# Performance work log

Hardware: AMD Instinct MI355X
Metric: run time of the kernel (lower is better)

The kernel has to match this reference:

```python
import jax, jax.numpy as jnp
import numpy as np

B, L, ENC, EMB, H, V = 64, 33, 512, 256, 512, 32000


def setup_inputs() -> dict:
    key = jax.random.key(0)
    ks = jax.random.split(key, 16)
    x = jax.random.normal(ks[0], (B, ENC), dtype=jnp.float32)
    padded_target = jax.random.randint(ks[1], (B, L), 0, V)
    target_lengths = jax.random.randint(ks[2], (B,), 2, L + 1)
    target_lengths = target_lengths.at[0].set(L)  # pin max length -> static step count
    s = 0.05
    return {
        "x": x,
        "padded_target": padded_target,
        "target_lengths": target_lengths,
        "embed": jax.random.normal(ks[3], (V, EMB), dtype=jnp.float32) * s,
        "W_h0": jax.random.normal(ks[4], (H, ENC), dtype=jnp.float32) * s,
        "b_h0": jnp.zeros((H,), jnp.float32),
        "W_c0": jax.random.normal(ks[5], (H, ENC), dtype=jnp.float32) * s,
        "b_c0": jnp.zeros((H,), jnp.float32),
        "W_ih": jax.random.normal(ks[6], (4 * H, ENC + EMB), dtype=jnp.float32) * s,
        "W_hh": jax.random.normal(ks[7], (4 * H, H), dtype=jnp.float32) * s,
        "b_ih": jnp.zeros((4 * H,), jnp.float32),
        "b_hh": jnp.zeros((4 * H,), jnp.float32),
        "W_out": jax.random.normal(ks[8], (V, H), dtype=jnp.float32) * s,
        "b_out": jnp.zeros((V,), jnp.float32),
    }


def reference(x, padded_target, target_lengths, embed, W_h0, b_h0, W_c0, b_c0,
              W_ih, W_hh, b_ih, b_hh, W_out, b_out):
    # sort by length, descending (packed-sequence ordering)
    sorted_indices = jnp.argsort(-target_lengths)
    x = x[sorted_indices]                      # [B, ENC]
    tgt = padded_target[sorted_indices]        # [B, L]
    lens = target_lengths[sorted_indices] - 1  # decode steps per row
    emb = embed[tgt]                           # [B, L, EMB]

    h = x @ W_h0.T + b_h0                      # context-initialized state
    c = x @ W_c0.T + b_c0
    T = padded_target.shape[1] - 1             # static max steps (max len pinned to L)

    def step(carry, inp):
        h, c = carry
        e_t, t = inp
        active = (lens > t)[:, None]           # rows still decoding (prefix, sorted)
        g = jnp.concatenate([x, e_t], axis=1) @ W_ih.T + b_ih + h @ W_hh.T + b_hh
        i, f, gg, o = jnp.split(g, 4, axis=1)  # torch LSTMCell gate order i,f,g,o
        c_new = jax.nn.sigmoid(f) * c + jax.nn.sigmoid(i) * jnp.tanh(gg)
        h_new = jax.nn.sigmoid(o) * jnp.tanh(c_new)
        h = jnp.where(active, h_new, h)        # inactive rows keep frozen state
        c = jnp.where(active, c_new, c)
        pred = jnp.where(active, h_new @ W_out.T + b_out, 0.0)  # dropout p=0
        return (h, c), pred

    (_, _), preds = jax.lax.scan(
        step, (h, c), (jnp.transpose(emb[:, :T], (1, 0, 2)), jnp.arange(T)))
    prediction = jnp.transpose(preds, (1, 0, 2))  # [B, T, V]
    return prediction, sorted_indices
```

## Files before the change

kernel.cpp:

```cpp
#include <hip/hip_runtime.h>

typedef __attribute__((ext_vector_type(8))) short short8;
typedef __attribute__((ext_vector_type(8))) unsigned short ushort8;
typedef __attribute__((ext_vector_type(4))) float f32x4;
typedef __attribute__((ext_vector_type(4))) unsigned short ushort4v;

#define DEV __device__ __forceinline__

DEV unsigned short f2bf(float f) {
  unsigned int u = __float_as_uint(f);
  u += 0x7fffu + ((u >> 16) & 1u);
  return (unsigned short)(u >> 16);
}
DEV float sigm(float x) { return 1.f / (1.f + __expf(-x)); }
DEV float tanh_(float x) { return 1.f - 2.f / (1.f + __expf(2.f * x)); }

typedef __attribute__((address_space(1))) const void* as1cv;
typedef __attribute__((address_space(3))) void* as3v;
DEV void gll16(const void* g, void* l) {
  __builtin_amdgcn_global_load_lds((as1cv)g, (as3v)l, 16, 0, 0);
}

__global__ void __launch_bounds__(256) k_sort(const float* __restrict__ x,
    const int* __restrict__ ptar, const int* __restrict__ tlen,
    int* __restrict__ sidx, int* __restrict__ lens, int* __restrict__ tok,
    float* __restrict__ xs, float* __restrict__ tail) {
  __shared__ int ss[64];
  int tid = threadIdx.x;
  if (tid < 64) {
    int li = tlen[tid];
    int rank = 0;
    for (int j = 0; j < 64; ++j) {
      int lj = tlen[j];
      rank += (lj > li || (lj == li && j < tid)) ? 1 : 0;
    }
    ss[rank] = tid;
  }
  __syncthreads();
  if (tid < 64) {
    int src = ss[tid];
    sidx[tid] = src;
    lens[tid] = tlen[src] - 1;
    tail[tid] = (float)src;
  }
  __syncthreads();
  for (int idx = tid; idx < 32 * 64; idx += 256) {
    int t = idx >> 6, b = idx & 63;
    tok[idx] = ptar[ss[b] * 33 + t];
  }
  for (int idx = tid; idx < 64 * 512; idx += 256) {
    int b = idx >> 9;
    xs[idx] = x[ss[b] * 512 + (idx & 511)];
  }
}

__global__ void __launch_bounds__(256) k_convmany(
    const float* __restrict__ W_h0, const float* __restrict__ W_c0,
    const float* __restrict__ W_ih, const float* __restrict__ W_hh,
    const float* __restrict__ xs,
    unsigned short* __restrict__ Wpro, unsigned short* __restrict__ Wihb2,
    unsigned short* __restrict__ Whb, unsigned short* __restrict__ xsb) {
  long long g = (long long)(blockIdx.x * 256 + threadIdx.x) * 8;
  const float* src;
  unsigned short* dst;
  if (g < 262144) {
    src = W_h0 + g; dst = Wpro + g;
  } else if (g < 524288) {
    long long l = g - 262144; src = W_c0 + l; dst = Wpro + 262144 + l;
  } else if (g < 1572864) {
    long long l = g - 524288;
    long long r = l >> 9, c = l & 511;
    src = W_ih + r * 768 + c; dst = Wpro + 524288 + l;
  } else if (g < 2097152) {
    long long l = g - 1572864;
    long long r = l >> 8, c = l & 255;
    src = W_ih + r * 768 + 512 + c; dst = Wihb2 + l;
  } else if (g < 3145728) {
    long long l = g - 2097152; src = W_hh + l; dst = Whb + l;
  } else {
    long long l = g - 3145728; src = xs + l; dst = xsb + l;
  }
  float4 v0 = *(const float4*)src, v1 = *(const float4*)(src + 4);
  ushort8 o;
  o[0] = f2bf(v0.x); o[1] = f2bf(v0.y); o[2] = f2bf(v0.z); o[3] = f2bf(v0.w);
  o[4] = f2bf(v1.x); o[5] = f2bf(v1.y); o[6] = f2bf(v1.z); o[7] = f2bf(v1.w);
  *(ushort8*)dst = o;
}

__global__ void __launch_bounds__(256) k_conv(const float* __restrict__ W,
    unsigned short* __restrict__ Wb) {
  size_t i = (size_t)(blockIdx.x * 256 + threadIdx.x) * 4;
  float4 v = *(const float4*)(W + i);
  ushort4v o;
  o.x = f2bf(v.x); o.y = f2bf(v.y); o.z = f2bf(v.z); o.w = f2bf(v.w);
  *(ushort4v*)(Wb + i) = o;
}

__global__ void __launch_bounds__(256) k_pro(const unsigned short* __restrict__ xsb,
    const unsigned short* __restrict__ Wpro, const float* __restrict__ b_h0,
    const float* __restrict__ b_c0, const float* __restrict__ b_ih,
    const float* __restrict__ b_hh, unsigned short* __restrict__ h0b,
    float* __restrict__ c, float* __restrict__ gx) {
  int tid = threadIdx.x, lane = tid & 63, w = tid >> 6;
  int n0 = blockIdx.x * 64 + w * 16;
  int lr = lane & 15, lk = lane >> 4;
  f32x4 acc[4];
#pragma unroll
  for (int i = 0; i < 4; ++i) acc[i] = (f32x4){0.f, 0.f, 0.f, 0.f};
  const unsigned short* B = Wpro + (size_t)(n0 + lr) * 512 + lk * 8;
  const unsigned short* A = xsb + (size_t)lr * 512 + lk * 8;
#pragma unroll
  for (int ks = 0; ks < 16; ++ks) {
    short8 bfr = *(const short8*)(B + ks * 32);
#pragma unroll
    for (int mi = 0; mi < 4; ++mi) {
      short8 af = *(const short8*)(A + mi * 16 * 512 + ks * 32);
      acc[mi] = __builtin_amdgcn_mfma_f32_16x16x32_bf16(af, bfr, acc[mi], 0, 0, 0);
    }
  }
  int n = n0 + lr;
#pragma unroll
  for (int mi = 0; mi < 4; ++mi)
#pragma unroll
    for (int r = 0; r < 4; ++r) {
      int b = mi * 16 + lk * 4 + r;
      float v = acc[mi][r];
      if (n < 512) {
        h0b[b * 512 + n] = f2bf(v + b_h0[n]);
      } else if (n < 1024) {
        int u = n - 512;
        c[b * 512 + u] = v + b_c0[u];
      } else {
        int j = n - 1024;
        gx[(size_t)b * 2048 + j] = v + b_ih[j] + b_hh[j];
      }
    }
}

__global__ void __launch_bounds__(256) k_emb(const int* __restrict__ tok,
    const float* __restrict__ embed, unsigned short* __restrict__ Eb) {
  int gid = blockIdx.x * 256 + threadIdx.x;
  int row = gid >> 5, c8 = (gid & 31) * 8;
  const float* src = embed + (size_t)tok[row] * 256 + c8;
  float4 v0 = *(const float4*)src, v1 = *(const float4*)(src + 4);
  ushort8 o;
  o[0] = f2bf(v0.x); o[1] = f2bf(v0.y); o[2] = f2bf(v0.z); o[3] = f2bf(v0.w);
  o[4] = f2bf(v1.x); o[5] = f2bf(v1.y); o[6] = f2bf(v1.z); o[7] = f2bf(v1.w);
  *(ushort8*)(Eb + (size_t)row * 256 + c8) = o;
}

__global__ void __launch_bounds__(256) k_ga2(const unsigned short* __restrict__ Eb,
    const unsigned short* __restrict__ Wb2, const float* __restrict__ gx,
    float* __restrict__ GA) {
  __shared__ alignas(16) char ldsbuf[32768];
  char* ldsA = ldsbuf;
  char* ldsB = ldsbuf + 16384;
  int bid = blockIdx.x;
  int mt = bid & 15, nt = bid >> 4;
  int m0 = mt * 128, n0 = nt * 128;
  int tid = threadIdx.x, lane = tid & 63, w = tid >> 6;
  int wm = w >> 1, wn = w & 1;
  f32x4 acc[4][4];
#pragma unroll
  for (int a = 0; a < 4; ++a)
#pragma unroll
    for (int bq = 0; bq < 4; ++bq) acc[a][bq] = (f32x4){0.f, 0.f, 0.f, 0.f};
  const unsigned short* Arow = Eb + (size_t)m0 * 256;
  const unsigned short* Brow = Wb2 + (size_t)n0 * 256;
  for (int kt = 0; kt < 4; ++kt) {
    int k0 = kt * 64;
    if (kt) __syncthreads();
#pragma unroll
    for (int j = 0; j < 4; ++j) {
      int ci = j * 256 + w * 64 + lane;
      int r = ci >> 3;
      int clog = ((ci & 7) << 4) ^ ((r & 7) << 4);
      int ldst = (j * 256 + w * 64) * 16;
      gll16((const char*)(Arow + (size_t)r * 256 + k0) + clog, ldsA + ldst);
      gll16((const char*)(Brow + (size_t)r * 256 + k0) + clog, ldsB + ldst);
    }
    __syncthreads();
#pragma unroll
    for (int kk = 0; kk < 2; ++kk) {
      short8 af[4], bf[4];
      int cb = kk * 64 + (lane >> 4) * 16;
#pragma unroll
      for (int i = 0; i < 4; ++i) {
        int ar = wm * 64 + i * 16 + (lane & 15);
        af[i] = *(const short8*)(ldsA + ar * 128 + (cb ^ ((ar & 7) << 4)));
        int br = wn * 64 + i * 16 + (lane & 15);
        bf[i] = *(const short8*)(ldsB + br * 128 + (cb ^ ((br & 7) << 4)));
      }
#pragma unroll
      for (int mi = 0; mi < 4; ++mi)
#pragma unroll
        for (int ni = 0; ni < 4; ++ni)
          acc[mi][ni] = __builtin_amdgcn_mfma_f32_16x16x32_bf16(
              af[mi], bf[ni], acc[mi][ni], 0, 0, 0);
    }
  }
#pragma unroll
  for (int mi = 0; mi < 4; ++mi) {
    int mb = m0 + wm * 64 + mi * 16 + ((lane >> 4) << 2);
#pragma unroll
    for (int r = 0; r < 4; ++r) {
      int m = mb + r;
#pragma unroll
      for (int ni = 0; ni < 4; ++ni) {
        int j = n0 + wn * 64 + ni * 16 + (lane & 15);
        GA[(size_t)m * 2048 + j] = acc[mi][ni][r] + gx[(size_t)(m & 63) * 2048 + j];
      }
    }
  }
}

__global__ void __launch_bounds__(256) k_step2(
    const unsigned short* __restrict__ hin, unsigned short* __restrict__ hout,
    float* __restrict__ c, const float* __restrict__ GA,
    const unsigned short* __restrict__ Whb, const int* __restrict__ lens,
    unsigned short* __restrict__ Hm, int t) {
  __shared__ float Gs[4][32][16];
  int tid = threadIdx.x, lane = tid & 63, g = tid >> 6;
  int bk = blockIdx.x, mh = bk & 1, u0 = (bk >> 1) * 16;
  int lr = lane & 15, lk = lane >> 4;
  f32x4 acc[2];
  acc[0] = (f32x4){0.f, 0.f, 0.f, 0.f};
  acc[1] = (f32x4){0.f, 0.f, 0.f, 0.f};
  const unsigned short* B = Whb + (size_t)(g * 512 + u0 + lr) * 512 + lk * 8;
  const unsigned short* A = hin + (size_t)(mh * 32 + lr) * 512 + lk * 8;
#pragma unroll
  for (int ks = 0; ks < 16; ++ks) {
    short8 bfr = *(const short8*)(B + ks * 32);
    short8 a0 = *(const short8*)(A + ks * 32);
    short8 a1 = *(const short8*)(A + 16 * 512 + ks * 32);
    acc[0] = __builtin_amdgcn_mfma_f32_16x16x32_bf16(a0, bfr, acc[0], 0, 0, 0);
    acc[1] = __builtin_amdgcn_mfma_f32_16x16x32_bf16(a1, bfr, acc[1], 0, 0, 0);
  }
  const float* gab = GA + (size_t)(t * 64 + mh * 32) * 2048 + g * 512 + u0 + lr;
#pragma unroll
  for (int mi = 0; mi < 2; ++mi)
#pragma unroll
    for (int r = 0; r < 4; ++r) {
      int rl = mi * 16 + lk * 4 + r;
      Gs[g][rl][lr] = acc[mi][r] + gab[(size_t)rl * 2048];
    }
  __syncthreads();
#pragma unroll
  for (int cell = tid; cell < 512; cell += 256) {
    int row = cell >> 4, uc = cell & 15;
    int b = mh * 32 + row, u = u0 + uc;
    float fi = Gs[0][row][uc], ff = Gs[1][row][uc];
    float fg = Gs[2][row][uc], fo = Gs[3][row][uc];
    float cold = c[b * 512 + u];
    float cn = sigm(ff) * cold + sigm(fi) * tanh_(fg);
    float hn = sigm(fo) * tanh_(cn);
    bool act = lens[b] > t;
    if (act) c[b * 512 + u] = cn;
    unsigned short hb = f2bf(hn);
    hout[b * 512 + u] = act ? hb : hin[b * 512 + u];
    Hm[((size_t)b * 32 + t) * 512 + u] = act ? hb : (unsigned short)0;
  }
}

__global__ void __launch_bounds__(256) k_gemm(const unsigned short* __restrict__ Hm,
    const unsigned short* __restrict__ Wb, const float* __restrict__ b_out,
    const int* __restrict__ lens, float* __restrict__ out) {
  __shared__ alignas(16) char ldsbuf[32768];
  char* ldsA = ldsbuf;
  char* ldsB = ldsbuf + 16384;
  int bid = blockIdx.x;
  int mt = bid & 15, nt = bid >> 4;
  int m0 = mt * 128, n0 = nt * 128;
  int tid = threadIdx.x, lane = tid & 63, w = tid >> 6;
  int wm = w >> 1, wn = w & 1;
  f32x4 acc[4][4];
#pragma unroll
  for (int a = 0; a < 4; ++a)
#pragma unroll
    for (int bq = 0; bq < 4; ++bq) acc[a][bq] = (f32x4){0.f, 0.f, 0.f, 0.f};
  const unsigned short* Arow = Hm + (size_t)m0 * 512;
  const unsigned short* Brow = Wb + (size_t)n0 * 512;
  for (int kt = 0; kt < 8; ++kt) {
    int k0 = kt * 64;
    if (kt) __syncthreads();
#pragma unroll
    for (int j = 0; j < 4; ++j) {
      int ci = j * 256 + w * 64 + lane;
      int r = ci >> 3;
      int clog = ((ci & 7) << 4) ^ ((r & 7) << 4);
      int ldst = (j * 256 + w * 64) * 16;
      gll16((const char*)(Arow + (size_t)r * 512 + k0) + clog, ldsA + ldst);
      gll16((const char*)(Brow + (size_t)r * 512 + k0) + clog, ldsB + ldst);
    }
    __syncthreads();
#pragma unroll
    for (int kk = 0; kk < 2; ++kk) {
      short8 af[4], bf[4];
      int cb = kk * 64 + (lane >> 4) * 16;
#pragma unroll
      for (int i = 0; i < 4; ++i) {
        int ar = wm * 64 + i * 16 + (lane & 15);
        af[i] = *(const short8*)(ldsA + ar * 128 + (cb ^ ((ar & 7) << 4)));
        int br = wn * 64 + i * 16 + (lane & 15);
        bf[i] = *(const short8*)(ldsB + br * 128 + (cb ^ ((br & 7) << 4)));
      }
#pragma unroll
      for (int mi = 0; mi < 4; ++mi)
#pragma unroll
        for (int ni = 0; ni < 4; ++ni)
          acc[mi][ni] = __builtin_amdgcn_mfma_f32_16x16x32_bf16(
              af[mi], bf[ni], acc[mi][ni], 0, 0, 0);
    }
  }
#pragma unroll
  for (int mi = 0; mi < 4; ++mi) {
    int mb = m0 + wm * 64 + mi * 16 + ((lane >> 4) << 2);
#pragma unroll
    for (int r = 0; r < 4; ++r) {
      int m = mb + r;
      int b = m >> 5, t = m & 31;
      bool act = lens[b] > t;
      size_t orow = (size_t)m * 32000;
#pragma unroll
      for (int ni = 0; ni < 4; ++ni) {
        int n = n0 + wn * 64 + ni * 16 + (lane & 15);
        out[orow + n] = act ? (acc[mi][ni][r] + b_out[n]) : 0.f;
      }
    }
  }
}

extern "C" void kernel_launch(void* const* d_in, const int* in_sizes, int n_in,
                              void* d_out, int out_size, void* d_ws, size_t ws_size,
                              hipStream_t stream) {
  const float* x     = (const float*)d_in[0];
  const int*   ptar  = (const int*)d_in[1];
  const int*   tlen  = (const int*)d_in[2];
  const float* embed = (const float*)d_in[3];
  const float* W_h0  = (const float*)d_in[4];
  const float* b_h0  = (const float*)d_in[5];
  const float* W_c0  = (const float*)d_in[6];
  const float* b_c0  = (const float*)d_in[7];
  const float* W_ih  = (const float*)d_in[8];
  const float* W_hh  = (const float*)d_in[9];
  const float* b_ih  = (const float*)d_in[10];
  const float* b_hh  = (const float*)d_in[11];
  const float* W_out = (const float*)d_in[12];
  const float* b_out = (const float*)d_in[13];
  float* out = (float*)d_out;

  char* ws = (char*)d_ws;
  size_t off = 0;
  auto alloc = [&](size_t bytes) {
    void* p = ws + off;
    off += (bytes + 255) & ~(size_t)255;
    return p;
  };
  unsigned short* Wob = (unsigned short*)alloc(32000ull * 512 * 2);
  unsigned short* Hm  = (unsigned short*)alloc(2048ull * 512 * 2);
  float* xs   = (float*)alloc(64 * 512 * 4);
  unsigned short* h0b = (unsigned short*)alloc(64 * 512 * 2);
  unsigned short* h1b = (unsigned short*)alloc(64 * 512 * 2);
  float* cbuf = (float*)alloc(64 * 512 * 4);
  float* gx   = (float*)alloc(64 * 2048 * 4);
  int* sidx = (int*)alloc(64 * 4);
  int* lens = (int*)alloc(64 * 4);
  int* tok  = (int*)alloc(2048 * 4);

  float* GA = out;
  unsigned short* Wpro  = (unsigned short*)(out + 4194304);
  unsigned short* Wihb2 = (unsigned short*)(out + 4980736);
  unsigned short* Whb   = (unsigned short*)(out + 5242880);
  unsigned short* Eb    = (unsigned short*)(out + 5767168);
  unsigned short* xsb   = (unsigned short*)(out + 6029312);
  float* tail = out + 65536000;

  k_sort<<<1, 256, 0, stream>>>(x, ptar, tlen, sidx, lens, tok, xs, tail);
  k_convmany<<<1552, 256, 0, stream>>>(W_h0, W_c0, W_ih, W_hh, xs,
                                       Wpro, Wihb2, Whb, xsb);
  k_conv<<<16000, 256, 0, stream>>>(W_out, Wob);
  k_pro<<<48, 256, 0, stream>>>(xsb, Wpro, b_h0, b_c0, b_ih, b_hh, h0b, cbuf, gx);
  k_emb<<<256, 256, 0, stream>>>(tok, embed, Eb);
  k_ga2<<<256, 256, 0, stream>>>(Eb, Wihb2, gx, GA);

  unsigned short* hb[2] = {h0b, h1b};
  for (int t = 0; t < 32; ++t)
    k_step2<<<64, 256, 0, stream>>>(hb[t & 1], hb[(t + 1) & 1], cbuf, GA, Whb,
                                    lens, Hm, t);

  k_gemm<<<4000, 256, 0, stream>>>(Hm, Wob, b_out, lens, out);
  (void)in_sizes; (void)n_in; (void)out_size; (void)ws_size;
}
```

Measured before the change: 448.9 us.

## Fuse LSTM recurrence into one persistent kernel with a grid barrier and overlapped W_out conversion

Replaces the 32 per-timestep launches of the recurrent step with one persistent kernel of 64 worker blocks. The blocks sync across steps through a global atomic barrier, with counters reset in the sort kernel. Each block keeps its W_hh fragments and cell state in registers across all steps. Extra blocks in the same grid convert W_out to bf16 alongside the recurrence, replacing the separate conversion launch. This removes launch overhead and repeated weight loads, but depends on all worker blocks being co-resident. It also stops writing zeros into Hm for inactive rows, relying on the GEMM's length masking.

```diff
diff --git a/kernel.cpp b/kernel.cpp
--- a/kernel.cpp
+++ b/kernel.cpp
@@ -3,7 +3,6 @@
 typedef __attribute__((ext_vector_type(8))) short short8;
 typedef __attribute__((ext_vector_type(8))) unsigned short ushort8;
 typedef __attribute__((ext_vector_type(4))) float f32x4;
-typedef __attribute__((ext_vector_type(4))) unsigned short ushort4v;
 
 #define DEV __device__ __forceinline__
 
@@ -24,9 +23,10 @@
 __global__ void __launch_bounds__(256) k_sort(const float* __restrict__ x,
     const int* __restrict__ ptar, const int* __restrict__ tlen,
     int* __restrict__ sidx, int* __restrict__ lens, int* __restrict__ tok,
-    float* __restrict__ xs, float* __restrict__ tail) {
+    float* __restrict__ xs, float* __restrict__ tail, int* __restrict__ bar) {
   __shared__ int ss[64];
   int tid = threadIdx.x;
+  if (tid < 32) bar[tid] = 0;
   if (tid < 64) {
     int li = tlen[tid];
     int rank = 0;
@@ -87,15 +87,6 @@
   *(ushort8*)dst = o;
 }
 
-__global__ void __launch_bounds__(256) k_conv(const float* __restrict__ W,
-    unsigned short* __restrict__ Wb) {
-  size_t i = (size_t)(blockIdx.x * 256 + threadIdx.x) * 4;
-  float4 v = *(const float4*)(W + i);
-  ushort4v o;
-  o.x = f2bf(v.x); o.y = f2bf(v.y); o.z = f2bf(v.z); o.w = f2bf(v.w);
-  *(ushort4v*)(Wb + i) = o;
-}
-
 __global__ void __launch_bounds__(256) k_pro(const unsigned short* __restrict__ xsb,
     const unsigned short* __restrict__ Wpro, const float* __restrict__ b_h0,
     const float* __restrict__ b_c0, const float* __restrict__ b_ih,
@@ -214,51 +205,101 @@
   }
 }
 
-__global__ void __launch_bounds__(256) k_step2(
-    const unsigned short* __restrict__ hin, unsigned short* __restrict__ hout,
-    float* __restrict__ c, const float* __restrict__ GA,
+__global__ void __launch_bounds__(256) k_steps(
+    unsigned short* __restrict__ h0, unsigned short* __restrict__ h1,
+    const float* __restrict__ c0, const float* __restrict__ GA,
     const unsigned short* __restrict__ Whb, const int* __restrict__ lens,
-    unsigned short* __restrict__ Hm, int t) {
+    unsigned short* __restrict__ Hm, int* __restrict__ bar,
+    const float* __restrict__ W_out, unsigned short* __restrict__ Wob) {
+  int tid = threadIdx.x, bid = blockIdx.x;
+  if (bid >= 64) {
+    for (long long i = ((long long)(bid - 64) * 256 + tid) * 8; i < 16384000LL;
+         i += 192LL * 256 * 8) {
+      float4 v0 = *(const float4*)(W_out + i);
+      float4 v1 = *(const float4*)(W_out + i + 4);
+      ushort8 o;
+      o[0] = f2bf(v0.x); o[1] = f2bf(v0.y); o[2] = f2bf(v0.z); o[3] = f2bf(v0.w);
+      o[4] = f2bf(v1.x); o[5] = f2bf(v1.y); o[6] = f2bf(v1.z); o[7] = f2bf(v1.w);
+      *(ushort8*)(Wob + i) = o;
+    }
+    return;
+  }
   __shared__ float Gs[4][32][16];
-  int tid = threadIdx.x, lane = tid & 63, g = tid >> 6;
-  int bk = blockIdx.x, mh = bk & 1, u0 = (bk >> 1) * 16;
-  int lr = lane & 15, lk = lane >> 4;
-  f32x4 acc[2];
-  acc[0] = (f32x4){0.f, 0.f, 0.f, 0.f};
-  acc[1] = (f32x4){0.f, 0.f, 0.f, 0.f};
-  const unsigned short* B = Whb + (size_t)(g * 512 + u0 + lr) * 512 + lk * 8;
-  const unsigned short* A = hin + (size_t)(mh * 32 + lr) * 512 + lk * 8;
-#pragma unroll
-  for (int ks = 0; ks < 16; ++ks) {
-    short8 bfr = *(const short8*)(B + ks * 32);
-    short8 a0 = *(const short8*)(A + ks * 32);
-    short8 a1 = *(const short8*)(A + 16 * 512 + ks * 32);
-    acc[0] = __builtin_amdgcn_mfma_f32_16x16x32_bf16(a0, bfr, acc[0], 0, 0, 0);
-    acc[1] = __builtin_amdgcn_mfma_f32_16x16x32_bf16(a1, bfr, acc[1], 0, 0, 0);
-  }
-  const float* gab = GA + (size_t)(t * 64 + mh * 32) * 2048 + g * 512 + u0 + lr;
-#pragma unroll
-  for (int mi = 0; mi < 2; ++mi)
+  int lane = tid & 63, g = tid >> 6, lr = lane & 15, lk = lane >> 4;
+  int mh = bid & 1, u0 = (bid >> 1) * 16;
+
+  short8 Bf[16];
+  {
+    const unsigned short* Bp = Whb + (size_t)(g * 512 + u0 + lr) * 512 + lk * 8;
+#pragma unroll
+    for (int ks = 0; ks < 16; ++ks) Bf[ks] = *(const short8*)(Bp + ks * 32);
+  }
+  int row0 = tid >> 4, uc = tid & 15;
+  int b0 = mh * 32 + row0, b1 = b0 + 16;
+  int u = u0 + uc;
+  float cr0 = c0[b0 * 512 + u], cr1 = c0[b1 * 512 + u];
+  int len0 = lens[b0], len1 = lens[b1];
+
+  for (int t = 0; t < 32; ++t) {
+    const unsigned short* hin = (t & 1) ? h1 : h0;
+    unsigned short* hout = (t & 1) ? h0 : h1;
+    const float* gab = GA + ((size_t)t * 64 + mh * 32) * 2048 + g * 512 + u0 + lr;
+    float gv0[4], gv1[4];
 #pragma unroll
     for (int r = 0; r < 4; ++r) {
-      int rl = mi * 16 + lk * 4 + r;
-      Gs[g][rl][lr] = acc[mi][r] + gab[(size_t)rl * 2048];
-    }
-  __syncthreads();
-#pragma unroll
-  for (int cell = tid; cell < 512; cell += 256) {
-    int row = cell >> 4, uc = cell & 15;
-    int b = mh * 32 + row, u = u0 + uc;
-    float fi = Gs[0][row][uc], ff = Gs[1][row][uc];
-    float fg = Gs[2][row][uc], fo = Gs[3][row][uc];
-    float cold = c[b * 512 + u];
-    float cn = sigm(ff) * cold + sigm(fi) * tanh_(fg);
-    float hn = sigm(fo) * tanh_(cn);
-    bool act = lens[b] > t;
-    if (act) c[b * 512 + u] = cn;
-    unsigned short hb = f2bf(hn);
-    hout[b * 512 + u] = act ? hb : hin[b * 512 + u];
-    Hm[((size_t)b * 32 + t) * 512 + u] = act ? hb : (unsigned short)0;
+      gv0[r] = gab[(size_t)(lk * 4 + r) * 2048];
+      gv1[r] = gab[(size_t)(16 + lk * 4 + r) * 2048];
+    }
+    const unsigned short* Ap = hin + (size_t)(mh * 32 + lr) * 512 + lk * 8;
+    f32x4 ac0 = {0.f, 0.f, 0.f, 0.f}, ac1 = {0.f, 0.f, 0.f, 0.f};
+#pragma unroll
+    for (int ks = 0; ks < 16; ++ks) {
+      short8 a0 = *(const short8*)(Ap + ks * 32);
+      short8 a1 = *(const short8*)(Ap + 8192 + ks * 32);
+      ac0 = __builtin_amdgcn_mfma_f32_16x16x32_bf16(a0, Bf[ks], ac0, 0, 0, 0);
+      ac1 = __builtin_amdgcn_mfma_f32_16x16x32_bf16(a1, Bf[ks], ac1, 0, 0, 0);
+    }
+#pragma unroll
+    for (int r = 0; r < 4; ++r) {
+      Gs[g][lk * 4 + r][lr] = ac0[r] + gv0[r];
+      Gs[g][16 + lk * 4 + r][lr] = ac1[r] + gv1[r];
+    }
+    __syncthreads();
+    {
+      float fi = Gs[0][row0][uc], ff = Gs[1][row0][uc];
+      float fg = Gs[2][row0][uc], fo = Gs[3][row0][uc];
+      float cn = sigm(ff) * cr0 + sigm(fi) * tanh_(fg);
+      float hn = sigm(fo) * tanh_(cn);
+      bool act = len0 > t;
+      cr0 = act ? cn : cr0;
+      unsigned short hbv = f2bf(hn);
+      unsigned short holdv = hin[b0 * 512 + u];
+      hout[b0 * 512 + u] = act ? hbv : holdv;
+      if (act) Hm[((size_t)b0 * 32 + t) * 512 + u] = hbv;
+    }
+    {
+      float fi = Gs[0][row0 + 16][uc], ff = Gs[1][row0 + 16][uc];
+      float fg = Gs[2][row0 + 16][uc], fo = Gs[3][row0 + 16][uc];
+      float cn = sigm(ff) * cr1 + sigm(fi) * tanh_(fg);
+      float hn = sigm(fo) * tanh_(cn);
+      bool act = len1 > t;
+      cr1 = act ? cn : cr1;
+      unsigned short hbv = f2bf(hn);
+      unsigned short holdv = hin[b1 * 512 + u];
+      hout[b1 * 512 + u] = act ? hbv : holdv;
+      if (act) Hm[((size_t)b1 * 32 + t) * 512 + u] = hbv;
+    }
+    __syncthreads();
+    if (tid == 0) {
+      __threadfence();
+      __hip_atomic_fetch_add(&bar[t], 1, __ATOMIC_ACQ_REL,
+                             __HIP_MEMORY_SCOPE_AGENT);
+      while (__hip_atomic_load(&bar[t], __ATOMIC_ACQUIRE,
+                               __HIP_MEMORY_SCOPE_AGENT) < 64)
+        __builtin_amdgcn_s_sleep(1);
+      __threadfence();
+    }
+    __syncthreads();
   }
 }
 
@@ -366,6 +407,7 @@
   int* sidx = (int*)alloc(64 * 4);
   int* lens = (int*)alloc(64 * 4);
   int* tok  = (int*)alloc(2048 * 4);
+  int* bar  = (int*)alloc(32 * 4);
 
   float* GA = out;
   unsigned short* Wpro  = (unsigned short*)(out + 4194304);
@@ -375,18 +417,15 @@
   unsigned short* xsb   = (unsigned short*)(out + 6029312);
   float* tail = out + 65536000;
 
-  k_sort<<<1, 256, 0, stream>>>(x, ptar, tlen, sidx, lens, tok, xs, tail);
+  k_sort<<<1, 256, 0, stream>>>(x, ptar, tlen, sidx, lens, tok, xs, tail, bar);
   k_convmany<<<1552, 256, 0, stream>>>(W_h0, W_c0, W_ih, W_hh, xs,
                                        Wpro, Wihb2, Whb, xsb);
-  k_conv<<<16000, 256, 0, stream>>>(W_out, Wob);
   k_pro<<<48, 256, 0, stream>>>(xsb, Wpro, b_h0, b_c0, b_ih, b_hh, h0b, cbuf, gx);
   k_emb<<<256, 256, 0, stream>>>(tok, embed, Eb);
   k_ga2<<<256, 256, 0, stream>>>(Eb, Wihb2, gx, GA);
 
-  unsigned short* hb[2] = {h0b, h1b};
-  for (int t = 0; t < 32; ++t)
-    k_step2<<<64, 256, 0, stream>>>(hb[t & 1], hb[(t + 1) & 1], cbuf, GA, Whb,
-                                    lens, Hm, t);
+  k_steps<<<256, 256, 0, stream>>>(h0b, h1b, cbuf, GA, Whb, lens, Hm, bar,
+                                   W_out, Wob);
 
   k_gemm<<<4000, 256, 0, stream>>>(Hm, Wob, b_out, lens, out);
   (void)in_sizes; (void)n_in; (void)out_size; (void)ws_size;
```

After: 569.0 us. 26.8% more time.
